# Performance work log

Hardware: AMD Instinct MI355X
Metric: run time of the kernel (lower is better)

## Reference

```python
import jax, jax.numpy as jnp
import numpy as np

T, H, E, I, K = 4096, 1024, 16, 768, 8  # tokens, hidden, experts, intermediate, top_k


def setup_inputs() -> dict:
    key = jax.random.key(0)
    k0, k1, k2, k3, k4 = jax.random.split(key, 5)
    scale = 0.02
    return {
        "hidden_states": jax.random.normal(k0, (T, H), dtype=jnp.float32),
        "gate_w": jax.random.normal(k1, (H, E), dtype=jnp.float32) * scale,
        "w1": jax.random.normal(k2, (E, H, I), dtype=jnp.float32) * scale,  # gate proj
        "w3": jax.random.normal(k3, (E, H, I), dtype=jnp.float32) * scale,  # up proj
        "w2": jax.random.normal(k4, (E, I, H), dtype=jnp.float32) * scale,  # down proj
    }


def reference(hidden_states, gate_w, w1, w3, w2):
    x = hidden_states  # [T, H]
    # Router: replicated linear (no bias) -> softmax -> top-k -> renormalize
    router_logits = x @ gate_w  # [T, E]
    probs = jax.nn.softmax(router_logits.astype(jnp.float32), axis=-1)
    topk_w, topk_idx = jax.lax.top_k(probs, K)  # [T, K]
    topk_w = topk_w / jnp.sum(topk_w, axis=-1, keepdims=True)  # norm_topk_prob=True
    # Dense routing-weight matrix [T, E]: zero for non-selected experts
    dense_w = jnp.zeros((T, E), dtype=x.dtype)
    dense_w = dense_w.at[jnp.arange(T)[:, None], topk_idx].set(topk_w.astype(x.dtype))
    # SwiGLU experts, computed densely over experts and masked by routing weights
    h = jnp.einsum("th,ehi->tei", x, w1)  # [T, E, I]
    u = jnp.einsum("th,ehi->tei", x, w3)  # [T, E, I]
    act = jax.nn.silu(h) * u  # [T, E, I]
    out = jnp.einsum("tei,eih,te->th", act, w2, dense_w)  # weighted combine -> [T, H]
    return out
```

## Files before the change

### kernel.cpp

```cpp
#include <hip/hip_runtime.h>
#include <hip/hip_bf16.h>

#define T_ 4096
#define H_ 1024
#define E_ 16
#define I_ 768
#define EI_ 12288
#define KTOP 8
#define KSPLIT 3
#define KLEN 4096

typedef __attribute__((ext_vector_type(8))) short bf16x8;
typedef __attribute__((ext_vector_type(4))) float f32x4;

__device__ __forceinline__ unsigned short f2bf(float f) {
  unsigned u = __builtin_bit_cast(unsigned, f);
  u += 0x7fff + ((u >> 16) & 1);
  return (unsigned short)(u >> 16);
}

typedef __attribute__((address_space(3))) void lds_void;
typedef __attribute__((address_space(1))) void g_void;

__device__ __forceinline__ void gload_lds16(const void* g, void* l) {
  __builtin_amdgcn_global_load_lds((g_void*)g, (lds_void*)l, 16, 0, 0);
}

__global__ void router_kernel(const float* __restrict__ x,
                              const float* __restrict__ gate_w,
                              float* __restrict__ dense_w) {
  int t = blockIdx.x;
  int lane = threadIdx.x;
  int e = lane & 15;
  int chunk = lane >> 4;
  const float* xr = x + (size_t)t * H_;
  int h0 = chunk * 256;
  float partial = 0.f;
  for (int i = 0; i < 256; i += 4) {
    float4 xv = *reinterpret_cast<const float4*>(xr + h0 + i);
    partial += xv.x * gate_w[(size_t)(h0 + i    ) * E_ + e];
    partial += xv.y * gate_w[(size_t)(h0 + i + 1) * E_ + e];
    partial += xv.z * gate_w[(size_t)(h0 + i + 2) * E_ + e];
    partial += xv.w * gate_w[(size_t)(h0 + i + 3) * E_ + e];
  }
  partial += __shfl_xor(partial, 16);
  partial += __shfl_xor(partial, 32);
  float logit = partial;
  float m = logit;
  for (int d = 1; d < 16; d <<= 1) m = fmaxf(m, __shfl_xor(m, d));
  float p = __expf(logit - m);
  int base = lane & ~15;
  int rank = 0;
  for (int j = 0; j < 16; ++j) {
    float pj = __shfl(p, base + j);
    rank += (pj > p) || (pj == p && j < e);
  }
  bool sel = rank < KTOP;
  float contrib = sel ? p : 0.f;
  float s = contrib;
  for (int d = 1; d < 16; d <<= 1) s += __shfl_xor(s, d);
  float w = sel ? p / s : 0.f;
  if (lane < 16) dense_w[(size_t)t * E_ + lane] = w;
}

__global__ void cast_x_kernel(const float* __restrict__ x,
                              unsigned short* __restrict__ xb) {
  int idx = blockIdx.x * blockDim.x + threadIdx.x;
  float4 v = reinterpret_cast<const float4*>(x)[idx];
  ushort4 o;
  o.x = f2bf(v.x); o.y = f2bf(v.y); o.z = f2bf(v.z); o.w = f2bf(v.w);
  *reinterpret_cast<ushort4*>(xb + (size_t)idx * 4) = o;
}

__global__ void transpose_w13_kernel(const float* __restrict__ w1,
                                     const float* __restrict__ w3,
                                     unsigned short* __restrict__ w1t,
                                     unsigned short* __restrict__ w3t) {
  __shared__ float tile[64][65];
  int i0 = blockIdx.x * 64;
  int h0 = blockIdx.y * 64;
  int e = blockIdx.z & 15;
  const float* src = (blockIdx.z < 16 ? w1 : w3) + (size_t)e * H_ * I_;
  unsigned short* dst = (blockIdx.z < 16 ? w1t : w3t) + (size_t)e * I_ * H_;
  int tx = threadIdx.x & 63, ty = threadIdx.x >> 6;
  for (int r = 0; r < 64; r += 4)
    tile[ty + r][tx] = src[(size_t)(h0 + ty + r) * I_ + i0 + tx];
  __syncthreads();
  for (int r = 0; r < 64; r += 4) {
    int i = ty + r;
    dst[(size_t)(i0 + i) * H_ + h0 + tx] = f2bf(tile[tx][i]);
  }
}

__global__ void transpose_w2_kernel(const float* __restrict__ w2,
                                    unsigned short* __restrict__ w2t) {
  __shared__ float tile[64][65];
  int h0 = blockIdx.x * 64;
  int i0 = blockIdx.y * 64;
  int e = blockIdx.z;
  const float* src = w2 + (size_t)e * I_ * H_;
  int tx = threadIdx.x & 63, ty = threadIdx.x >> 6;
  for (int r = 0; r < 64; r += 4)
    tile[ty + r][tx] = src[(size_t)(i0 + ty + r) * H_ + h0 + tx];
  __syncthreads();
  for (int r = 0; r < 64; r += 4) {
    int h = ty + r;
    w2t[(size_t)(h0 + h) * EI_ + (size_t)e * I_ + i0 + tx] = f2bf(tile[tx][h]);
  }
}

__global__ __launch_bounds__(256) void moe_up_kernel(
    const unsigned short* __restrict__ xb,
    const unsigned short* __restrict__ w1t,
    const unsigned short* __restrict__ w3t,
    const float* __restrict__ dense_w,
    unsigned short* __restrict__ act) {
  __shared__ __align__(16) unsigned short Asm[128 * 32];
  __shared__ __align__(16) unsigned short B1sm[64 * 32];
  __shared__ __align__(16) unsigned short B3sm[64 * 32];
  __shared__ float rw_sm[128];

  const int e = blockIdx.z;
  const int row0 = blockIdx.x * 128;
  const int col0 = blockIdx.y * 64;
  const int tid = threadIdx.x;
  const int lane = tid & 63;
  const int w = tid >> 6;
  const int wm = w >> 1, wn = w & 1;

  if (tid < 128) rw_sm[tid] = dense_w[(size_t)(row0 + tid) * E_ + e];

  const int r_in_chunk = lane >> 2;
  const int kpart = (lane & 3) * 8;

  const unsigned short* Abase  = xb  + (size_t)row0 * H_;
  const unsigned short* B1base = w1t + ((size_t)e * I_ + col0) * H_;
  const unsigned short* B3base = w3t + ((size_t)e * I_ + col0) * H_;

  f32x4 acc1[4][2] = {};
  f32x4 acc2[4][2] = {};

  const int lrow = lane & 15;
  const int lk = (lane >> 4) * 8;

  for (int k0 = 0; k0 < H_; k0 += 32) {
    for (int i = 0; i < 4; ++i) {
      int c = w * 4 + i;
      if (c < 8) {
        int row = c * 16 + r_in_chunk;
        gload_lds16(Abase + (size_t)row * H_ + k0 + kpart, &Asm[c * 512]);
      } else if (c < 12) {
        int row = (c - 8) * 16 + r_in_chunk;
        gload_lds16(B1base + (size_t)row * H_ + k0 + kpart, &B1sm[(c - 8) * 512]);
      } else {
        int row = (c - 12) * 16 + r_in_chunk;
        gload_lds16(B3base + (size_t)row * H_ + k0 + kpart, &B3sm[(c - 12) * 512]);
      }
    }
    __syncthreads();
    bf16x8 af[4], b1f[2], b3f[2];
    for (int m = 0; m < 4; ++m)
      af[m] = *reinterpret_cast<const bf16x8*>(&Asm[(wm * 64 + m * 16 + lrow) * 32 + lk]);
    for (int n = 0; n < 2; ++n) {
      b1f[n] = *reinterpret_cast<const bf16x8*>(&B1sm[(wn * 32 + n * 16 + lrow) * 32 + lk]);
      b3f[n] = *reinterpret_cast<const bf16x8*>(&B3sm[(wn * 32 + n * 16 + lrow) * 32 + lk]);
    }
    for (int m = 0; m < 4; ++m)
      for (int n = 0; n < 2; ++n) {
        acc1[m][n] = __builtin_amdgcn_mfma_f32_16x16x32_bf16(af[m], b1f[n], acc1[m][n], 0, 0, 0);
        acc2[m][n] = __builtin_amdgcn_mfma_f32_16x16x32_bf16(af[m], b3f[n], acc2[m][n], 0, 0, 0);
      }
    __syncthreads();
  }

  const int crow = (lane >> 4) * 4;
  const int ccol = lane & 15;
  for (int m = 0; m < 4; ++m)
    for (int n = 0; n < 2; ++n)
      for (int r = 0; r < 4; ++r) {
        int rl = wm * 64 + m * 16 + crow + r;
        int cl = wn * 32 + n * 16 + ccol;
        float hv = acc1[m][n][r];
        float uv = acc2[m][n][r];
        float a = (hv / (1.f + __expf(-hv))) * uv * rw_sm[rl];
        act[(size_t)(row0 + rl) * EI_ + (size_t)e * I_ + col0 + cl] = f2bf(a);
      }
}

__global__ __launch_bounds__(256) void moe_down_kernel(
    const unsigned short* __restrict__ act,
    const unsigned short* __restrict__ w2t,
    float* __restrict__ dout) {
  __shared__ __align__(16) unsigned short Asm[128 * 32];
  __shared__ __align__(16) unsigned short Bsm[128 * 32];

  const int row0 = blockIdx.x * 128;
  const int col0 = blockIdx.y * 128;
  const int ks = blockIdx.z;
  const int tid = threadIdx.x;
  const int lane = tid & 63;
  const int w = tid >> 6;
  const int wm = w >> 1, wn = w & 1;

  const int r_in_chunk = lane >> 2;
  const int kpart = (lane & 3) * 8;

  const unsigned short* Abase = act + (size_t)row0 * EI_;
  const unsigned short* Bbase = w2t + (size_t)col0 * EI_;

  f32x4 acc[4][4] = {};

  const int lrow = lane & 15;
  const int lk = (lane >> 4) * 8;

  const int kbeg = ks * KLEN;
  for (int k0 = kbeg; k0 < kbeg + KLEN; k0 += 32) {
    for (int i = 0; i < 2; ++i) {
      int c = w * 2 + i;
      int row = c * 16 + r_in_chunk;
      gload_lds16(Abase + (size_t)row * EI_ + k0 + kpart, &Asm[c * 512]);
      gload_lds16(Bbase + (size_t)row * EI_ + k0 + kpart, &Bsm[c * 512]);
    }
    __syncthreads();
    bf16x8 af[4], bf[4];
    for (int m = 0; m < 4; ++m)
      af[m] = *reinterpret_cast<const bf16x8*>(&Asm[(wm * 64 + m * 16 + lrow) * 32 + lk]);
    for (int n = 0; n < 4; ++n)
      bf[n] = *reinterpret_cast<const bf16x8*>(&Bsm[(wn * 64 + n * 16 + lrow) * 32 + lk]);
    for (int m = 0; m < 4; ++m)
      for (int n = 0; n < 4; ++n)
        acc[m][n] = __builtin_amdgcn_mfma_f32_16x16x32_bf16(af[m], bf[n], acc[m][n], 0, 0, 0);
    __syncthreads();
  }

  float* dbase = dout + (size_t)ks * T_ * H_;
  const int crow = (lane >> 4) * 4;
  const int ccol = lane & 15;
  for (int m = 0; m < 4; ++m)
    for (int n = 0; n < 4; ++n)
      for (int r = 0; r < 4; ++r) {
        int rl = wm * 64 + m * 16 + crow + r;
        int cl = wn * 64 + n * 16 + ccol;
        dbase[(size_t)(row0 + rl) * H_ + col0 + cl] = acc[m][n][r];
      }
}

__global__ void reduce_kernel(const float* __restrict__ dout,
                              float* __restrict__ out) {
  int idx = blockIdx.x * blockDim.x + threadIdx.x;
  const float4* a = reinterpret_cast<const float4*>(dout);
  const float4* b = a + (size_t)T_ * H_ / 4;
  const float4* c = b + (size_t)T_ * H_ / 4;
  float4 va = a[idx], vb = b[idx], vc = c[idx];
  float4 o;
  o.x = va.x + vb.x + vc.x;
  o.y = va.y + vb.y + vc.y;
  o.z = va.z + vb.z + vc.z;
  o.w = va.w + vb.w + vc.w;
  reinterpret_cast<float4*>(out)[idx] = o;
}

extern "C" void kernel_launch(void* const* d_in, const int* in_sizes, int n_in,
                              void* d_out, int out_size, void* d_ws, size_t ws_size,
                              hipStream_t stream) {
  const float* x      = (const float*)d_in[0];
  const float* gate_w = (const float*)d_in[1];
  const float* w1     = (const float*)d_in[2];
  const float* w3     = (const float*)d_in[3];
  const float* w2     = (const float*)d_in[4];
  float* out = (float*)d_out;

  char* ws = (char*)d_ws;
  float* dense_w      = (float*)ws;
  unsigned short* xb  = (unsigned short*)(ws + 262144);
  unsigned short* w1t = xb  + (size_t)T_ * H_;
  unsigned short* w3t = w1t + (size_t)E_ * I_ * H_;
  unsigned short* w2t = w3t + (size_t)E_ * I_ * H_;
  unsigned short* act = w2t + (size_t)H_ * EI_;
  float* dout = (float*)w1t;

  router_kernel<<<T_, 64, 0, stream>>>(x, gate_w, dense_w);
  cast_x_kernel<<<(T_ * H_ / 4) / 256, 256, 0, stream>>>(x, xb);
  transpose_w13_kernel<<<dim3(I_ / 64, H_ / 64, 32), 256, 0, stream>>>(w1, w3, w1t, w3t);
  transpose_w2_kernel<<<dim3(H_ / 64, I_ / 64, E_), 256, 0, stream>>>(w2, w2t);
  moe_up_kernel<<<dim3(T_ / 128, I_ / 64, E_), 256, 0, stream>>>(xb, w1t, w3t, dense_w, act);
  moe_down_kernel<<<dim3(T_ / 128, H_ / 128, KSPLIT), 256, 0, stream>>>(act, w2t, dout);
  reduce_kernel<<<(T_ * H_ / 4) / 256, 256, 0, stream>>>(dout, out);
}
```

Before: 733.8 us.

## Switch dense MoE to sparse token-gathered grouped GEMM with atomic scatter

The router now builds per-expert token lists with atomics, and the up and down GEMMs run only on the tokens routed to each expert. Previously every expert was computed for every token and masked. Gathered rows are loaded directly into LDS, and the down projection scatters results into the output with float atomicAdd, which removes the split-K partial buffers and the reduce kernel. This cuts the expert FLOPs roughly in half (8 of 16 experts per token). In exchange it adds two memsets, a serial offsets kernel, padding tiles, atomic contention on the output, and a summation order that is no longer deterministic.

```diff
diff --git a/kernel.cpp b/kernel.cpp
--- a/kernel.cpp
+++ b/kernel.cpp
@@ -5,10 +5,9 @@
 #define H_ 1024
 #define E_ 16
 #define I_ 768
-#define EI_ 12288
 #define KTOP 8
-#define KSPLIT 3
-#define KLEN 4096
+#define MAXSLOT 4096
+#define ACT_ROWS 34816
 
 typedef __attribute__((ext_vector_type(8))) short bf16x8;
 typedef __attribute__((ext_vector_type(4))) float f32x4;
@@ -28,7 +27,9 @@
 
 __global__ void router_kernel(const float* __restrict__ x,
                               const float* __restrict__ gate_w,
-                              float* __restrict__ dense_w) {
+                              int* __restrict__ cnt,
+                              int* __restrict__ tok_list,
+                              float* __restrict__ rw_list) {
   int t = blockIdx.x;
   int lane = threadIdx.x;
   int e = lane & 15;
@@ -60,7 +61,23 @@
   float s = contrib;
   for (int d = 1; d < 16; d <<= 1) s += __shfl_xor(s, d);
   float w = sel ? p / s : 0.f;
-  if (lane < 16) dense_w[(size_t)t * E_ + lane] = w;
+  if (lane < 16 && sel) {
+    int slot = atomicAdd(&cnt[e], 1);
+    tok_list[e * MAXSLOT + slot] = t;
+    rw_list[e * MAXSLOT + slot] = w;
+  }
+}
+
+__global__ void offsets_kernel(const int* __restrict__ cnt,
+                               int* __restrict__ off,
+                               int* __restrict__ ntiles) {
+  int acc = 0;
+  for (int e = 0; e < E_; ++e) {
+    off[e] = acc;
+    int nt = (cnt[e] + 127) >> 7;
+    ntiles[e] = nt;
+    acc += nt << 7;
+  }
 }
 
 __global__ void cast_x_kernel(const float* __restrict__ x,
@@ -93,7 +110,7 @@
 }
 
 __global__ void transpose_w2_kernel(const float* __restrict__ w2,
-                                    unsigned short* __restrict__ w2t) {
+                                    unsigned short* __restrict__ w2te) {
   __shared__ float tile[64][65];
   int h0 = blockIdx.x * 64;
   int i0 = blockIdx.y * 64;
@@ -105,7 +122,7 @@
   __syncthreads();
   for (int r = 0; r < 64; r += 4) {
     int h = ty + r;
-    w2t[(size_t)(h0 + h) * EI_ + (size_t)e * I_ + i0 + tx] = f2bf(tile[tx][h]);
+    w2te[((size_t)e * H_ + h0 + h) * I_ + i0 + tx] = f2bf(tile[tx][h]);
   }
 }
 
@@ -113,27 +130,46 @@
     const unsigned short* __restrict__ xb,
     const unsigned short* __restrict__ w1t,
     const unsigned short* __restrict__ w3t,
-    const float* __restrict__ dense_w,
-    unsigned short* __restrict__ act) {
+    const int* __restrict__ tok_list,
+    const float* __restrict__ rw_list,
+    const int* __restrict__ off,
+    const int* __restrict__ ntiles,
+    unsigned short* __restrict__ act_g) {
+  const int e = blockIdx.z;
+  const int tile = blockIdx.x;
+  if (tile >= ntiles[e]) return;
+
   __shared__ __align__(16) unsigned short Asm[128 * 32];
   __shared__ __align__(16) unsigned short B1sm[64 * 32];
   __shared__ __align__(16) unsigned short B3sm[64 * 32];
+  __shared__ int tok_sm[128];
   __shared__ float rw_sm[128];
 
-  const int e = blockIdx.z;
-  const int row0 = blockIdx.x * 128;
   const int col0 = blockIdx.y * 64;
   const int tid = threadIdx.x;
   const int lane = tid & 63;
   const int w = tid >> 6;
   const int wm = w >> 1, wn = w & 1;
-
-  if (tid < 128) rw_sm[tid] = dense_w[(size_t)(row0 + tid) * E_ + e];
+  const int slot0 = off[e] + tile * 128;
+
+  if (tid < 128) {
+    int li = e * MAXSLOT + tile * 128 + tid;
+    tok_sm[tid] = tok_list[li];
+    rw_sm[tid] = rw_list[li];
+  }
+  __syncthreads();
 
   const int r_in_chunk = lane >> 2;
   const int kpart = (lane & 3) * 8;
 
-  const unsigned short* Abase  = xb  + (size_t)row0 * H_;
+  const unsigned short* asrc[4];
+  if (w < 2) {
+#pragma unroll
+    for (int i = 0; i < 4; ++i) {
+      int row = (w * 4 + i) * 16 + r_in_chunk;
+      asrc[i] = xb + (size_t)tok_sm[row] * H_ + kpart;
+    }
+  }
   const unsigned short* B1base = w1t + ((size_t)e * I_ + col0) * H_;
   const unsigned short* B3base = w3t + ((size_t)e * I_ + col0) * H_;
 
@@ -144,17 +180,21 @@
   const int lk = (lane >> 4) * 8;
 
   for (int k0 = 0; k0 < H_; k0 += 32) {
-    for (int i = 0; i < 4; ++i) {
-      int c = w * 4 + i;
-      if (c < 8) {
-        int row = c * 16 + r_in_chunk;
-        gload_lds16(Abase + (size_t)row * H_ + k0 + kpart, &Asm[c * 512]);
-      } else if (c < 12) {
-        int row = (c - 8) * 16 + r_in_chunk;
-        gload_lds16(B1base + (size_t)row * H_ + k0 + kpart, &B1sm[(c - 8) * 512]);
-      } else {
-        int row = (c - 12) * 16 + r_in_chunk;
-        gload_lds16(B3base + (size_t)row * H_ + k0 + kpart, &B3sm[(c - 12) * 512]);
+    if (w < 2) {
+#pragma unroll
+      for (int i = 0; i < 4; ++i)
+        gload_lds16(asrc[i] + k0, &Asm[(w * 4 + i) * 512]);
+    } else if (w == 2) {
+#pragma unroll
+      for (int i = 0; i < 4; ++i) {
+        int row = i * 16 + r_in_chunk;
+        gload_lds16(B1base + (size_t)row * H_ + k0 + kpart, &B1sm[i * 512]);
+      }
+    } else {
+#pragma unroll
+      for (int i = 0; i < 4; ++i) {
+        int row = i * 16 + r_in_chunk;
+        gload_lds16(B3base + (size_t)row * H_ + k0 + kpart, &B3sm[i * 512]);
       }
     }
     __syncthreads();
@@ -183,43 +223,50 @@
         float hv = acc1[m][n][r];
         float uv = acc2[m][n][r];
         float a = (hv / (1.f + __expf(-hv))) * uv * rw_sm[rl];
-        act[(size_t)(row0 + rl) * EI_ + (size_t)e * I_ + col0 + cl] = f2bf(a);
+        act_g[(size_t)(slot0 + rl) * I_ + col0 + cl] = f2bf(a);
       }
 }
 
 __global__ __launch_bounds__(256) void moe_down_kernel(
-    const unsigned short* __restrict__ act,
-    const unsigned short* __restrict__ w2t,
-    float* __restrict__ dout) {
+    const unsigned short* __restrict__ act_g,
+    const unsigned short* __restrict__ w2te,
+    const int* __restrict__ tok_list,
+    const int* __restrict__ off,
+    const int* __restrict__ ntiles,
+    float* __restrict__ out) {
+  const int e = blockIdx.z;
+  const int tile = blockIdx.x;
+  if (tile >= ntiles[e]) return;
+
   __shared__ __align__(16) unsigned short Asm[128 * 32];
   __shared__ __align__(16) unsigned short Bsm[128 * 32];
-
-  const int row0 = blockIdx.x * 128;
+  __shared__ int tok_sm[128];
+
   const int col0 = blockIdx.y * 128;
-  const int ks = blockIdx.z;
   const int tid = threadIdx.x;
   const int lane = tid & 63;
   const int w = tid >> 6;
   const int wm = w >> 1, wn = w & 1;
 
+  if (tid < 128) tok_sm[tid] = tok_list[e * MAXSLOT + tile * 128 + tid];
+
   const int r_in_chunk = lane >> 2;
   const int kpart = (lane & 3) * 8;
 
-  const unsigned short* Abase = act + (size_t)row0 * EI_;
-  const unsigned short* Bbase = w2t + (size_t)col0 * EI_;
+  const unsigned short* Abase = act_g + (size_t)(off[e] + tile * 128) * I_;
+  const unsigned short* Bbase = w2te + ((size_t)e * H_ + col0) * I_;
 
   f32x4 acc[4][4] = {};
 
   const int lrow = lane & 15;
   const int lk = (lane >> 4) * 8;
 
-  const int kbeg = ks * KLEN;
-  for (int k0 = kbeg; k0 < kbeg + KLEN; k0 += 32) {
+  for (int k0 = 0; k0 < I_; k0 += 32) {
     for (int i = 0; i < 2; ++i) {
       int c = w * 2 + i;
       int row = c * 16 + r_in_chunk;
-      gload_lds16(Abase + (size_t)row * EI_ + k0 + kpart, &Asm[c * 512]);
-      gload_lds16(Bbase + (size_t)row * EI_ + k0 + kpart, &Bsm[c * 512]);
+      gload_lds16(Abase + (size_t)row * I_ + k0 + kpart, &Asm[c * 512]);
+      gload_lds16(Bbase + (size_t)row * I_ + k0 + kpart, &Bsm[c * 512]);
     }
     __syncthreads();
     bf16x8 af[4], bf[4];
@@ -233,7 +280,6 @@
     __syncthreads();
   }
 
-  float* dbase = dout + (size_t)ks * T_ * H_;
   const int crow = (lane >> 4) * 4;
   const int ccol = lane & 15;
   for (int m = 0; m < 4; ++m)
@@ -241,23 +287,8 @@
       for (int r = 0; r < 4; ++r) {
         int rl = wm * 64 + m * 16 + crow + r;
         int cl = wn * 64 + n * 16 + ccol;
-        dbase[(size_t)(row0 + rl) * H_ + col0 + cl] = acc[m][n][r];
-      }
-}
-
-__global__ void reduce_kernel(const float* __restrict__ dout,
-                              float* __restrict__ out) {
-  int idx = blockIdx.x * blockDim.x + threadIdx.x;
-  const float4* a = reinterpret_cast<const float4*>(dout);
-  const float4* b = a + (size_t)T_ * H_ / 4;
-  const float4* c = b + (size_t)T_ * H_ / 4;
-  float4 va = a[idx], vb = b[idx], vc = c[idx];
-  float4 o;
-  o.x = va.x + vb.x + vc.x;
-  o.y = va.y + vb.y + vc.y;
-  o.z = va.z + vb.z + vc.z;
-  o.w = va.w + vb.w + vc.w;
-  reinterpret_cast<float4*>(out)[idx] = o;
+        atomicAdd(&out[(size_t)tok_sm[rl] * H_ + col0 + cl], acc[m][n][r]);
+      }
 }
 
 extern "C" void kernel_launch(void* const* d_in, const int* in_sizes, int n_in,
@@ -270,20 +301,28 @@
   const float* w2     = (const float*)d_in[4];
   float* out = (float*)d_out;
 
-  char* ws = (char*)d_ws;
-  float* dense_w      = (float*)ws;
-  unsigned short* xb  = (unsigned short*)(ws + 262144);
-  unsigned short* w1t = xb  + (size_t)T_ * H_;
-  unsigned short* w3t = w1t + (size_t)E_ * I_ * H_;
-  unsigned short* w2t = w3t + (size_t)E_ * I_ * H_;
-  unsigned short* act = w2t + (size_t)H_ * EI_;
-  float* dout = (float*)w1t;
-
-  router_kernel<<<T_, 64, 0, stream>>>(x, gate_w, dense_w);
+  int* ctrl     = (int*)d_ws;
+  int* cnt      = ctrl;
+  int* off      = ctrl + 16;
+  int* ntiles   = ctrl + 32;
+  int* tok_list = ctrl + 64;
+  float* rw_list = (float*)(tok_list + E_ * MAXSLOT);
+  unsigned short* xb   = (unsigned short*)(rw_list + E_ * MAXSLOT);
+  unsigned short* w1t  = xb  + (size_t)T_ * H_;
+  unsigned short* w3t  = w1t + (size_t)E_ * I_ * H_;
+  unsigned short* w2te = w3t + (size_t)E_ * I_ * H_;
+  unsigned short* act_g = w2te + (size_t)E_ * H_ * I_;
+
+  hipMemsetAsync(d_ws, 0, (64 + 2 * E_ * MAXSLOT) * sizeof(int), stream);
+  hipMemsetAsync(d_out, 0, (size_t)T_ * H_ * sizeof(float), stream);
+
+  router_kernel<<<T_, 64, 0, stream>>>(x, gate_w, cnt, tok_list, rw_list);
+  offsets_kernel<<<1, 1, 0, stream>>>(cnt, off, ntiles);
   cast_x_kernel<<<(T_ * H_ / 4) / 256, 256, 0, stream>>>(x, xb);
   transpose_w13_kernel<<<dim3(I_ / 64, H_ / 64, 32), 256, 0, stream>>>(w1, w3, w1t, w3t);
-  transpose_w2_kernel<<<dim3(H_ / 64, I_ / 64, E_), 256, 0, stream>>>(w2, w2t);
-  moe_up_kernel<<<dim3(T_ / 128, I_ / 64, E_), 256, 0, stream>>>(xb, w1t, w3t, dense_w, act);
-  moe_down_kernel<<<dim3(T_ / 128, H_ / 128, KSPLIT), 256, 0, stream>>>(act, w2t, dout);
-  reduce_kernel<<<(T_ * H_ / 4) / 256, 256, 0, stream>>>(dout, out);
-}
+  transpose_w2_kernel<<<dim3(H_ / 64, I_ / 64, E_), 256, 0, stream>>>(w2, w2te);
+  moe_up_kernel<<<dim3(32, I_ / 64, E_), 256, 0, stream>>>(
+      xb, w1t, w3t, tok_list, rw_list, off, ntiles, act_g);
+  moe_down_kernel<<<dim3(32, H_ / 128, E_), 256, 0, stream>>>(
+      act_g, w2te, tok_list, off, ntiles, out);
+}
```

After: 774.2 us. 5.5% more time.
